# Kernel optimization log

Hardware: AMD Instinct MI355X
Metric: run time of the kernel (lower is better)

The kernel has to match this reference:

```python
import jax, jax.numpy as jnp
import numpy as np

P, D, C, F, B = 8, 2, 64, 64, 2048  # properties, disjuncts/property, classes, features, batch
T = P * D


def _make_post_graphs():
    # Each disjunct is a sparse DAG over classes: edge (i, j) means y_i >= y_j required.
    rng = np.random.RandomState(0)
    g = (rng.rand(T, C, C) < 0.05).astype(np.int32)
    return jnp.asarray(np.triu(g, k=1))


def setup_inputs():
    key = jax.random.key(0)
    kx, ky = jax.random.split(key)
    return {
        "x": jax.random.normal(kx, (B, F), jnp.float32),
        "y": jax.random.normal(ky, (B, C), jnp.float32),
        "post_graphs": _make_post_graphs(),
    }


def _contains_cycle(graph):
    # Kahn peel: repeatedly delete in-degree-0 nodes; cycle iff nodes remain. graph: [B,C,C]
    gf = graph.astype(jnp.float32)
    def body(_, rem):
        indeg = jnp.einsum('bi,bij->bj', rem, gf)
        return jnp.where((rem > 0) & (indeg == 0), 0.0, rem)
    rem = jax.lax.fori_loop(0, C, body, jnp.ones(graph.shape[:2], jnp.float32))
    return jnp.any(rem > 0, axis=1)


def _topo_ranks(y, graph):
    # Priority topological sort: among in-degree-0 remaining nodes pick max-y first.
    # rank[b, c] = position of class c in the topological order.
    gf = graph.astype(jnp.float32)
    n = y.shape[0]
    rows = jnp.arange(n)
    def step(carry, r):
        rem, rank = carry
        indeg = jnp.einsum('bi,bij->bj', rem, gf)
        score = jnp.where((rem > 0) & (indeg == 0), y, -jnp.inf)
        idx = jnp.argmax(score, axis=1)
        rank = rank.at[rows, idx].set(r)
        rem = rem * (1.0 - jax.nn.one_hot(idx, C, dtype=jnp.float32))
        return (rem, rank), None
    init = (jnp.ones((n, C), jnp.float32), jnp.zeros((n, C), jnp.int32))
    (_, rank), _ = jax.lax.scan(step, init, jnp.arange(C))
    return rank


def _forward(x, y, post_graphs):
    n = y.shape[0]
    required = (x[:, :P] > 0.0).astype(jnp.int32)          # [B,P] precondition satisfaction
    # 'preserve' heuristic: order disjuncts by ascending violation of current y
    diff = jax.nn.relu(y[:, None, :] - y[:, :, None])       # [B,C,C] relu(y_j - y_i)
    viol = jnp.einsum('bij,tij->bt', diff, post_graphs.astype(jnp.float32)).reshape(n, P, D)
    order = jnp.argsort(jax.lax.stop_gradient(viol), axis=2)  # [B,P,D]
    # greedy disjunction solve: per property, first heuristic-ordered choice whose union is acyclic
    acc = jnp.zeros((n, C, C), jnp.int32)
    for p in range(P):
        cand = post_graphs[p * D:(p + 1) * D]               # [D,C,C]
        chosen = order[:, p, 0]
        found = jnp.zeros((n,), bool)
        for k in range(D):
            dk = order[:, p, k]
            test = jnp.maximum(acc, required[:, p, None, None] * cand[dk])
            ok = ~_contains_cycle(test)
            chosen = jnp.where(found, chosen, jnp.where(ok, dk, chosen))
            found = found | ok
        acc = jnp.maximum(acc, required[:, p, None, None] * cand[chosen])  # graph_union
    graph = acc                                              # [B,C,C] selected postcondition graph
    rank = _topo_ranks(jax.lax.stop_gradient(y), graph)
    y_desc = -jnp.sort(-y, axis=1)                           # descending values of y
    y_fixed = jnp.take_along_axis(y_desc, rank, axis=1)      # assign sorted values by topo order
    sat = jnp.all((graph == 0) | (y[:, :, None] >= y[:, None, :]), axis=(1, 2))
    y_rep = jnp.where(sat[:, None], y, y_fixed)              # keep y where already satisfied
    gb = graph > 0
    margin = jnp.sum(jnp.where(gb, jax.nn.relu(y_rep[:, None, :] - y_rep[:, :, None]), 0.0), axis=(1, 2))
    bot = jnp.where(margin > 0.0, jnp.max(y_rep, axis=1) + margin, -jnp.inf)
    return jnp.concatenate([y_rep, bot[:, None]], axis=1)    # [B, C+1]


def reference(x, y, post_graphs):
    return _forward(x, y, post_graphs)
```

## Files before the change

### kernel.cpp

```cpp
#include <hip/hip_runtime.h>
#include <hip/hip_bf16.h>
#include <float.h>


#define C_NODES 64
#define T_GRAPHS 16
#define P_PHASES 8
#define F_DIM 64
#define MAXE 160
#define KITER (MAXE / 4)

typedef unsigned long long u64;

__device__ __forceinline__ float finite_or_zero(float v) {
    unsigned u = __float_as_uint(v);
    return ((u & 0x7f800000u) == 0x7f800000u) ? 0.0f : v;
}

__global__ __launch_bounds__(64) void gor_prep_v8(
    const int* __restrict__ g, u64* __restrict__ mask,
    unsigned short* __restrict__ elist) {
    const int t = blockIdx.x;
    const int lane = threadIdx.x;

    const uint4* row = (const uint4*)(g + (t * C_NODES + lane) * C_NODES);
    u64 m = 0ull;
    #pragma unroll
    for (int q = 0; q < 16; ++q) {
        uint4 v = row[q];
        m |= ((u64)(v.x != 0u)) << (4 * q + 0);
        m |= ((u64)(v.y != 0u)) << (4 * q + 1);
        m |= ((u64)(v.z != 0u)) << (4 * q + 2);
        m |= ((u64)(v.w != 0u)) << (4 * q + 3);
    }
    mask[t * C_NODES + lane] = m;

    int cnt = __popcll(m);
    int incl = cnt;
    #pragma unroll
    for (int off = 1; off < 64; off <<= 1) {
        int v = __shfl_up(incl, off);
        if (lane >= off) incl += v;
    }
    const int excl = incl - cnt;
    const int tot = __shfl(incl, 63);

    u64 mm = m;
    int e = excl;
    while (mm) {
        int j = __builtin_ctzll(mm); mm &= mm - 1;
        if (e < MAXE)
            elist[(e >> 2) * 64 + 16 * (e & 3) + t] =
                (unsigned short)((lane << 8) | j);
        ++e;
    }
    for (int e2 = tot + lane; e2 < MAXE; e2 += 64)
        elist[(e2 >> 2) * 64 + 16 * (e2 & 3) + t] = 0;
}

__global__ __launch_bounds__(64) void gor_repair_v8(
    const float* __restrict__ x, const float* __restrict__ y,
    const u64* __restrict__ mask, const unsigned short* __restrict__ elist,
    float* __restrict__ out) {
    const int b = blockIdx.x;
    const int lane = threadIdx.x;

    __shared__ float y_s[C_NODES];
    __shared__ int perm[C_NODES];

    const float y_l = finite_or_zero(y[b * C_NODES + lane]);
    y_s[lane] = y_l;
    __syncthreads();

    const u64 req = __ballot((lane < P_PHASES) && (x[b * F_DIM + lane] > 0.0f));

    float vp = 0.0f;
    #pragma unroll
    for (int k = 0; k < KITER; ++k) {
        unsigned ev = elist[k * 64 + lane];
        float yi = y_s[ev >> 8];
        float yj = y_s[ev & 255u];
        float d = yj - yi;
        vp += (d > 0.0f) ? d : 0.0f;
    }
    vp += __shfl_xor(vp, 16);
    vp += __shfl_xor(vp, 32);

    const int p8 = lane & 7;
    const float va = __shfl(vp, 2 * p8);
    const float vb = __shfl(vp, 2 * p8 + 1);
    const u64 takeb = __ballot((lane < P_PHASES) && (vb < va));

    u64 accrow = 0ull;
    #pragma unroll
    for (int p = 0; p < P_PHASES; ++p) {
        if ((req >> p) & 1ull) {
            const int tsel = 2 * p + (int)((takeb >> p) & 1ull);
            accrow |= mask[tsel * C_NODES + lane];
        }
    }

    bool bad = false;
    #pragma unroll
    for (int j = 0; j < C_NODES; ++j)
        if (((accrow >> j) & 1ull) && (y_s[j] > y_l)) bad = true;
    const bool sat = (__all((int)(!bad)) != 0);

    if (sat) {
        out[b * (C_NODES + 1) + lane] = y_l;
    } else {
        int dpos = 0;
        #pragma unroll
        for (int j = 0; j < C_NODES; ++j) {
            float yj = y_s[j];
            dpos += (yj > y_l) || (yj == y_l && j < lane);
        }
        perm[dpos] = lane;
        __syncthreads();

        const int n = perm[lane];

        unsigned alo = (unsigned)__shfl((int)(unsigned)accrow, n);
        unsigned ahi = (unsigned)__shfl((int)(unsigned)(accrow >> 32), n);
        const u64 accD = ((u64)ahi << 32) | (u64)alo;

        u64 predD = 0ull;
        #pragma unroll
        for (int dd = 0; dd < C_NODES; ++dd) {
            int ndd = perm[dd];
            u64 bb = __ballot((int)((accD >> ndd) & 1ull));
            if (dd == lane) predD = bb;
        }

        u64 remD = ~0ull;
        int myrank = 0;
        for (int r = 0; r < C_NODES; ++r) {
            bool avail = ((remD >> lane) & 1ull) && ((predD & remD) == 0ull);
            u64 bb = __ballot(avail);
            int d = __builtin_ctzll(bb);
            if (d == lane) myrank = r;
            remD &= ~(1ull << d);
        }

        out[b * (C_NODES + 1) + n] = y_s[perm[myrank]];
    }

    if (lane == 0) out[b * (C_NODES + 1) + C_NODES] = 0.0f;
}

extern "C" void kernel_launch(void* const* d_in, const int* in_sizes, int n_in,
                              void* d_out, int out_size, void* d_ws, size_t ws_size,
                              hipStream_t stream) {
    const float* x = (const float*)d_in[0];
    const float* y = (const float*)d_in[1];
    const int* post_graphs = (const int*)d_in[2];
    float* out = (float*)d_out;

    const int B = in_sizes[1] / C_NODES;

    u64* mask = (u64*)d_ws;
    unsigned short* elist = (unsigned short*)((char*)d_ws + 8192);

    gor_prep_v8<<<T_GRAPHS, C_NODES, 0, stream>>>(post_graphs, mask, elist);
    gor_repair_v8<<<B, C_NODES, 0, stream>>>(x, y, mask, elist, out);
}
```

Before: 22.14 us.

## Derive satisfaction from violation sums and precompute transposed predecessor masks

The satisfaction check no longer builds the union adjacency row and scans 64 classes. It reuses the per-disjunct violation sums: the selected graph is satisfied if every required property's chosen disjunct has zero violation. The prep kernel now stores transposed (predecessor) masks, which removes the 64-step ballot transpose in the repair kernel. The topo loop tracks removed nodes in original index space via shuffles, and the mask loads now happen only on the unsatisfied path. The violation sums are computed with strict comparisons on relu differences, so equality to zero should match the original check. The added per-iteration shuffle in the rank loop is extra work.

```diff
diff --git a/kernel.cpp b/kernel.cpp
--- a/kernel.cpp
+++ b/kernel.cpp
@@ -17,8 +17,8 @@
     return ((u & 0x7f800000u) == 0x7f800000u) ? 0.0f : v;
 }
 
-__global__ __launch_bounds__(64) void gor_prep_v8(
-    const int* __restrict__ g, u64* __restrict__ mask,
+__global__ __launch_bounds__(64) void gor_prep_v9(
+    const int* __restrict__ g, u64* __restrict__ maskT,
     unsigned short* __restrict__ elist) {
     const int t = blockIdx.x;
     const int lane = threadIdx.x;
@@ -33,7 +33,14 @@
         m |= ((u64)(v.z != 0u)) << (4 * q + 2);
         m |= ((u64)(v.w != 0u)) << (4 * q + 3);
     }
-    mask[t * C_NODES + lane] = m;
+
+    u64 mt = 0ull;
+    #pragma unroll
+    for (int j = 0; j < C_NODES; ++j) {
+        u64 cm = __ballot((m >> j) & 1ull);
+        if (j == lane) mt = cm;
+    }
+    maskT[t * C_NODES + lane] = mt;
 
     int cnt = __popcll(m);
     int incl = cnt;
@@ -58,15 +65,15 @@
         elist[(e2 >> 2) * 64 + 16 * (e2 & 3) + t] = 0;
 }
 
-__global__ __launch_bounds__(64) void gor_repair_v8(
+__global__ __launch_bounds__(64) void gor_repair_v9(
     const float* __restrict__ x, const float* __restrict__ y,
-    const u64* __restrict__ mask, const unsigned short* __restrict__ elist,
+    const u64* __restrict__ maskT, const unsigned short* __restrict__ elist,
     float* __restrict__ out) {
     const int b = blockIdx.x;
     const int lane = threadIdx.x;
 
     __shared__ float y_s[C_NODES];
-    __shared__ int perm[C_NODES];
+    __shared__ int perm_s[C_NODES];
 
     const float y_l = finite_or_zero(y[b * C_NODES + lane]);
     y_s[lane] = y_l;
@@ -91,20 +98,10 @@
     const float vb = __shfl(vp, 2 * p8 + 1);
     const u64 takeb = __ballot((lane < P_PHASES) && (vb < va));
 
-    u64 accrow = 0ull;
-    #pragma unroll
-    for (int p = 0; p < P_PHASES; ++p) {
-        if ((req >> p) & 1ull) {
-            const int tsel = 2 * p + (int)((takeb >> p) & 1ull);
-            accrow |= mask[tsel * C_NODES + lane];
-        }
-    }
-
-    bool bad = false;
-    #pragma unroll
-    for (int j = 0; j < C_NODES; ++j)
-        if (((accrow >> j) & 1ull) && (y_s[j] > y_l)) bad = true;
-    const bool sat = (__all((int)(!bad)) != 0);
+    const float minv = ((takeb >> p8) & 1ull) ? vb : va;
+    const bool myok =
+        (lane >= P_PHASES) || !((req >> p8) & 1ull) || (minv == 0.0f);
+    const bool sat = (__all((int)myok) != 0);
 
     if (sat) {
         out[b * (C_NODES + 1) + lane] = y_l;
@@ -115,34 +112,39 @@
             float yj = y_s[j];
             dpos += (yj > y_l) || (yj == y_l && j < lane);
         }
-        perm[dpos] = lane;
+        perm_s[dpos] = lane;
         __syncthreads();
 
-        const int n = perm[lane];
+        const int n = perm_s[lane];
 
-        unsigned alo = (unsigned)__shfl((int)(unsigned)accrow, n);
-        unsigned ahi = (unsigned)__shfl((int)(unsigned)(accrow >> 32), n);
-        const u64 accD = ((u64)ahi << 32) | (u64)alo;
+        u64 predcol = 0ull;
+        #pragma unroll
+        for (int p = 0; p < P_PHASES; ++p) {
+            if ((req >> p) & 1ull) {
+                const int tsel = 2 * p + (int)((takeb >> p) & 1ull);
+                predcol |= maskT[tsel * C_NODES + lane];
+            }
+        }
+        unsigned plo = (unsigned)__shfl((int)(unsigned)predcol, n);
+        unsigned phi = (unsigned)__shfl((int)(unsigned)(predcol >> 32), n);
+        const u64 pred_n = ((u64)phi << 32) | (u64)plo;
 
-        u64 predD = 0ull;
-        #pragma unroll
-        for (int dd = 0; dd < C_NODES; ++dd) {
-            int ndd = perm[dd];
-            u64 bb = __ballot((int)((accD >> ndd) & 1ull));
-            if (dd == lane) predD = bb;
-        }
+        const float y_slot = __shfl(y_l, n);
 
-        u64 remD = ~0ull;
+        u64 remN = ~0ull;
+        bool my_rem = true;
         int myrank = 0;
         for (int r = 0; r < C_NODES; ++r) {
-            bool avail = ((remD >> lane) & 1ull) && ((predD & remD) == 0ull);
+            bool avail = my_rem && ((pred_n & remN) == 0ull);
             u64 bb = __ballot(avail);
             int d = __builtin_ctzll(bb);
             if (d == lane) myrank = r;
-            remD &= ~(1ull << d);
+            my_rem = my_rem && (d != lane);
+            int nch = __shfl(n, d);
+            remN &= ~(1ull << nch);
         }
 
-        out[b * (C_NODES + 1) + n] = y_s[perm[myrank]];
+        out[b * (C_NODES + 1) + n] = __shfl(y_slot, myrank);
     }
 
     if (lane == 0) out[b * (C_NODES + 1) + C_NODES] = 0.0f;
@@ -158,9 +160,9 @@
 
     const int B = in_sizes[1] / C_NODES;
 
-    u64* mask = (u64*)d_ws;
+    u64* maskT = (u64*)d_ws;
     unsigned short* elist = (unsigned short*)((char*)d_ws + 8192);
 
-    gor_prep_v8<<<T_GRAPHS, C_NODES, 0, stream>>>(post_graphs, mask, elist);
-    gor_repair_v8<<<B, C_NODES, 0, stream>>>(x, y, mask, elist, out);
+    gor_prep_v9<<<T_GRAPHS, C_NODES, 0, stream>>>(post_graphs, maskT, elist);
+    gor_repair_v9<<<B, C_NODES, 0, stream>>>(x, y, maskT, elist, out);
 }
```

After: 20.58 us. 7.0% less time.
